# Optimization experiments

Measured on AMD Instinct MI355X. Metric: run time of the kernel, lower is better.

The kernel has to match this reference:

```python
import jax, jax.numpy as jnp
import numpy as np

HEAD_DIM = 64
K = 3              # kernel_size
DILATION = 1
SCALE = HEAD_DIM ** (-0.5)
PAD = DILATION * (K - 1) // 2


def setup_inputs() -> dict:
    key = jax.random.key(0)
    kq, kk, kv = jax.random.split(key, 3)
    shape = (8, 512, 56, 56)  # B, d, H, W
    return {
        "q": jax.random.normal(kq, shape, dtype=jnp.float32),
        "k": jax.random.normal(kk, shape, dtype=jnp.float32),
        "v": jax.random.normal(kv, shape, dtype=jnp.float32),
    }


def _unfold(x, B, h, H, W):
    # torch nn.Unfold(kernel=K, dilation=1, padding=PAD, stride=1):
    # output [B, d*K*K, H*W] with (channel, kh, kw) channel-major ordering,
    # which matches lax.conv_general_dilated_patches output layout.
    p = jax.lax.conv_general_dilated_patches(
        x, (K, K), (1, 1), ((PAD, PAD), (PAD, PAD)),
        rhs_dilation=(DILATION, DILATION),
        dimension_numbers=("NCHW", "OIHW", "NCHW"),
    )  # [B, d*K*K, H, W]
    return p.reshape(B, h, HEAD_DIM, K * K, H * W)


def reference(q, k, v):
    B, d, H, W = q.shape
    h = d // HEAD_DIM  # number of heads
    # q -> [B, h, HW, head_dim]
    qr = q.reshape(B, h, HEAD_DIM, H * W).transpose(0, 1, 3, 2)
    ku = _unfold(k, B, h, H, W)  # [B, h, hd, K*K, HW]
    vu = _unfold(v, B, h, H, W)  # [B, h, hd, K*K, HW]
    # per-pixel local attention over the K*K window
    attn = jnp.einsum("bhpc,bhckp->bhpk", qr, ku) * SCALE  # [B,h,HW,K*K]
    attn = jax.nn.softmax(attn, axis=-1)
    out = jnp.einsum("bhpk,bhckp->bhpc", attn, vu)  # [B,h,HW,hd]
    # -> [B, HW, h, hd] -> [B, H, W, d]
    return out.transpose(0, 2, 1, 3).reshape(B, H, W, d)
```

## Files before the change

kernel.cpp:

```cpp
#include <hip/hip_runtime.h>


namespace {

constexpr int HD = 64, HH = 56, WW = 56, HW = HH * WW;
constexpr int CS = HW, DTOT = 512;
constexpr float SCALE = 0.125f;
constexpr int TSTR = 36;

__device__ __forceinline__ float tapLf(float v) {
  int i = __float_as_int(v);
  return __int_as_float(__builtin_amdgcn_update_dpp(i, i, 0x138, 0xF, 0xF, false));
}
__device__ __forceinline__ float tapRf(float v) {
  int i = __float_as_int(v);
  return __int_as_float(__builtin_amdgcn_update_dpp(i, i, 0x130, 0xF, 0xF, false));
}

__global__ __launch_bounds__(64, 4)
void adda_fwd(const float* __restrict__ qg, const float* __restrict__ kg,
              const float* __restrict__ vg, float* __restrict__ outg) {
  __shared__ float tbuf[56 * TSTR];

  int wg = (int)blockIdx.x;
  const int nwg = (int)gridDim.x;
  if ((nwg & 7) == 0) wg = (wg & 7) * (nwg >> 3) + (wg >> 3);

  const int bh  = wg / 56;
  const int rem = wg - bh * 56;
  const int pair = rem >> 1;
  const int h    = rem & 1;
  const int l    = (int)threadIdx.x;
  const int r    = l >> 5;
  const int xc   = l & 31;
  const int y    = pair * 2;
  const int yown = y + r;
  const int x    = h * 28 - 1 + xc;
  const int xg   = x < 0 ? 0 : (x > WW - 1 ? WW - 1 : x);
  const int yout = r ? (y + 2 > HH - 1 ? HH - 1 : y + 2)
                     : (y > 0 ? y - 1 : 0);

  const long base = (long)bh * HD * HW;
  const float* __restrict__ qp  = qg + base + (long)yown * WW + xg;
  const float* __restrict__ kop = kg + base + (long)yown * WW + xg;
  const float* __restrict__ kxp = kg + base + (long)yout * WW + xg;
  const float* __restrict__ vop = vg + base + (long)yown * WW + xg;
  const float* __restrict__ vxp = vg + base + (long)yout * WW + xg;

  float lg[9];
#pragma unroll
  for (int n = 0; n < 9; ++n) lg[n] = 0.f;

  float koA[8], kxA[8], qqA[8];
  float koB[8], kxB[8], qqB[8];
  float voA[8], vxA[8];
  float voB[8], vxB[8];

#define LOADK(S, cb)                                    \
  _Pragma("unroll") for (int i = 0; i < 8; ++i) {       \
    qq##S[i] = qp[((cb) + i) * CS];                     \
    ko##S[i] = kop[((cb) + i) * CS];                    \
    kx##S[i] = kxp[((cb) + i) * CS];                    \
  }
#define CONSK(S)                                        \
  _Pragma("unroll") for (int i = 0; i < 8; ++i) {       \
    const float swp = __shfl_xor(ko##S[i], 32);         \
    const float abv = r ? swp : kx##S[i];               \
    const float blw = r ? kx##S[i] : swp;               \
    const float own = ko##S[i];                         \
    const float qv  = qq##S[i];                         \
    lg[0] = fmaf(qv, tapLf(abv), lg[0]);                \
    lg[1] = fmaf(qv, abv,        lg[1]);                \
    lg[2] = fmaf(qv, tapRf(abv), lg[2]);                \
    lg[3] = fmaf(qv, tapLf(own), lg[3]);                \
    lg[4] = fmaf(qv, own,        lg[4]);                \
    lg[5] = fmaf(qv, tapRf(own), lg[5]);                \
    lg[6] = fmaf(qv, tapLf(blw), lg[6]);                \
    lg[7] = fmaf(qv, blw,        lg[7]);                \
    lg[8] = fmaf(qv, tapRf(blw), lg[8]);                \
  }
#define LOADV(S, cb)                                    \
  _Pragma("unroll") for (int i = 0; i < 8; ++i) {       \
    vo##S[i] = vop[((cb) + i) * CS];                    \
    vx##S[i] = vxp[((cb) + i) * CS];                    \
  }

  LOADK(A, 0);  LOADK(B, 8);
  CONSK(A); LOADK(A, 16);
  CONSK(B); LOADK(B, 24);
  CONSK(A); LOADK(A, 32);
  CONSK(B); LOADK(B, 40);
  CONSK(A); LOADK(A, 48);
  CONSK(B); LOADK(B, 56);
  CONSK(A); LOADV(A, 0);
  CONSK(B); LOADV(B, 8);

  const bool okt = r ? true : (y > 0);
  const bool okb = r ? (y + 2 < HH) : true;
  const bool okl = x > 0;
  const bool okr = x < WW - 1;
  const bool ok[9] = {okt && okl, okt, okt && okr,
                      okl,        true, okr,
                      okb && okl, okb, okb && okr};
  float w[9];
  float mx = 0.f;
#pragma unroll
  for (int n = 0; n < 9; ++n) { w[n] = ok[n] ? lg[n] * SCALE : 0.f; mx = fmaxf(mx, w[n]); }
  float sum = 0.f;
#pragma unroll
  for (int n = 0; n < 9; ++n) { w[n] = __expf(w[n] - mx); sum += w[n]; }
  const float inv = 1.f / sum;
#pragma unroll
  for (int n = 0; n < 9; ++n) w[n] = ok[n] ? w[n] * inv : 0.f;

  const bool pxv = (xc >= 1) && (xc <= 28);
  const int pxw = r * 28 + xc - 1;

#define CONSV(S, cb)                                    \
  {                                                     \
    float o[8];                                         \
    _Pragma("unroll") for (int i = 0; i < 8; ++i) {     \
      const float swp = __shfl_xor(vo##S[i], 32);       \
      const float abv = r ? swp : vx##S[i];             \
      const float blw = r ? vx##S[i] : swp;             \
      const float own = vo##S[i];                       \
      float a = w[0] * tapLf(abv);                      \
      a = fmaf(w[1], abv,        a);                    \
      a = fmaf(w[2], tapRf(abv), a);                    \
      a = fmaf(w[3], tapLf(own), a);                    \
      a = fmaf(w[4], own,        a);                    \
      a = fmaf(w[5], tapRf(own), a);                    \
      a = fmaf(w[6], tapLf(blw), a);                    \
      a = fmaf(w[7], blw,        a);                    \
      a = fmaf(w[8], tapRf(blw), a);                    \
      o[i] = a;                                         \
    }                                                   \
    if (pxv) {                                          \
      const int cl = (cb) & 31;                         \
      *(float4*)&tbuf[pxw * TSTR + cl]     = make_float4(o[0], o[1], o[2], o[3]); \
      *(float4*)&tbuf[pxw * TSTR + cl + 4] = make_float4(o[4], o[5], o[6], o[7]); \
    }                                                   \
  }

  float* __restrict__ ob =
      outg + ((long)(bh >> 3) * HW + (long)y * WW + h * 28) * DTOT + (bh & 7) * HD;

#define READOUT(ch0)                                    \
  _Pragma("unroll") for (int rr = 0; rr < 7; ++rr) {    \
    const int g = rr * 64 + l;                          \
    const int pw = g >> 3, slot = g & 7;                \
    const int pa = pw + ((pw >= 28) ? 28 : 0);          \
    const float4 tv = *(const float4*)&tbuf[pw * TSTR + slot * 4]; \
    *(float4*)(ob + (long)pa * DTOT + (ch0) + slot * 4) = tv;      \
  }

  CONSV(A, 0);  LOADV(A, 16);
  CONSV(B, 8);  LOADV(B, 24);
  CONSV(A, 16); LOADV(A, 32);
  CONSV(B, 24); LOADV(B, 40);
  READOUT(0);
  CONSV(A, 32); LOADV(A, 48);
  CONSV(B, 40); LOADV(B, 56);
  CONSV(A, 48);
  CONSV(B, 56);
  READOUT(32);

#undef LOADK
#undef CONSK
#undef LOADV
#undef CONSV
#undef READOUT
}

}

extern "C" void kernel_launch(void* const* d_in, const int* in_sizes, int n_in,
                              void* d_out, int out_size, void* d_ws, size_t ws_size,
                              hipStream_t stream) {
  const float* q = (const float*)d_in[0];
  const float* k = (const float*)d_in[1];
  const float* v = (const float*)d_in[2];
  float* out = (float*)d_out;

  const int BH = in_sizes[0] / (HD * HW);
  dim3 grid(BH * 56);
  adda_fwd<<<grid, 64, 0, stream>>>(q, k, v, out);
}
```

Baseline: 39.21 us.

## Compute two horizontal pixels per lane with float2 loads over full-width row pairs

Each lane now owns two adjacent pixels, loaded as float2 from three rows (above, own, below) of q/k/v. Each workgroup covers a full 56-pixel row pair instead of half-row tiles with halo lanes. This drops the redundant halo loads and the cross-half shuffle, and halves the grid. The cost is doubled accumulator and weight registers (18 logits) and lower occupancy, with launch bounds reduced to 2, plus 4 of every 32 lanes idle.

```diff
diff --git a/kernel.cpp b/kernel.cpp
--- a/kernel.cpp
+++ b/kernel.cpp
@@ -6,6 +6,7 @@
 constexpr int HD = 64, HH = 56, WW = 56, HW = HH * WW;
 constexpr int CS = HW, DTOT = 512;
 constexpr float SCALE = 0.125f;
+constexpr int NP   = HH / 2;
 constexpr int TSTR = 36;
 
 __device__ __forceinline__ float tapLf(float v) {
@@ -17,72 +18,88 @@
   return __int_as_float(__builtin_amdgcn_update_dpp(i, i, 0x130, 0xF, 0xF, false));
 }
 
-__global__ __launch_bounds__(64, 4)
+__global__ __launch_bounds__(64, 2)
 void adda_fwd(const float* __restrict__ qg, const float* __restrict__ kg,
               const float* __restrict__ vg, float* __restrict__ outg) {
-  __shared__ float tbuf[56 * TSTR];
+  __shared__ float tbuf[112 * TSTR];
 
   int wg = (int)blockIdx.x;
   const int nwg = (int)gridDim.x;
   if ((nwg & 7) == 0) wg = (wg & 7) * (nwg >> 3) + (wg >> 3);
 
-  const int bh  = wg / 56;
-  const int rem = wg - bh * 56;
-  const int pair = rem >> 1;
-  const int h    = rem & 1;
+  const int pair = wg % NP;
+  const int bh   = wg / NP;
   const int l    = (int)threadIdx.x;
   const int r    = l >> 5;
-  const int xc   = l & 31;
+  const int pl   = l & 31;
+  const int p    = pl < 28 ? pl : 27;
+  const bool act = pl < 28;
   const int y    = pair * 2;
   const int yown = y + r;
-  const int x    = h * 28 - 1 + xc;
-  const int xg   = x < 0 ? 0 : (x > WW - 1 ? WW - 1 : x);
-  const int yout = r ? (y + 2 > HH - 1 ? HH - 1 : y + 2)
-                     : (y > 0 ? y - 1 : 0);
+  const int x0   = 2 * p;
 
   const long base = (long)bh * HD * HW;
-  const float* __restrict__ qp  = qg + base + (long)yown * WW + xg;
-  const float* __restrict__ kop = kg + base + (long)yown * WW + xg;
-  const float* __restrict__ kxp = kg + base + (long)yout * WW + xg;
-  const float* __restrict__ vop = vg + base + (long)yown * WW + xg;
-  const float* __restrict__ vxp = vg + base + (long)yout * WW + xg;
-
-  float lg[9];
-#pragma unroll
-  for (int n = 0; n < 9; ++n) lg[n] = 0.f;
-
-  float koA[8], kxA[8], qqA[8];
-  float koB[8], kxB[8], qqB[8];
-  float voA[8], vxA[8];
-  float voB[8], vxB[8];
+  const int rA = (yown > 0) ? yown - 1 : 0;
+  const int rC = (yown < HH - 1) ? yown + 1 : HH - 1;
+
+  const float* __restrict__ qp  = qg + base + (long)yown * WW + x0;
+  const float* __restrict__ kap = kg + base + (long)rA * WW + x0;
+  const float* __restrict__ kbp = kg + base + (long)yown * WW + x0;
+  const float* __restrict__ kcp = kg + base + (long)rC * WW + x0;
+  const float* __restrict__ vap = vg + base + (long)rA * WW + x0;
+  const float* __restrict__ vbp = vg + base + (long)yown * WW + x0;
+  const float* __restrict__ vcp = vg + base + (long)rC * WW + x0;
+
+  float lg[18];
+#pragma unroll
+  for (int n = 0; n < 18; ++n) lg[n] = 0.f;
+
+  float2 qA[8], aA[8], bA[8], cA[8];
+  float2 qB[8], aB[8], bB[8], cB[8];
 
 #define LOADK(S, cb)                                    \
   _Pragma("unroll") for (int i = 0; i < 8; ++i) {       \
-    qq##S[i] = qp[((cb) + i) * CS];                     \
-    ko##S[i] = kop[((cb) + i) * CS];                    \
-    kx##S[i] = kxp[((cb) + i) * CS];                    \
+    const int co = ((cb) + i) * CS;                     \
+    q##S[i] = *(const float2*)(qp + co);                \
+    a##S[i] = *(const float2*)(kap + co);               \
+    b##S[i] = *(const float2*)(kbp + co);               \
+    c##S[i] = *(const float2*)(kcp + co);               \
   }
 #define CONSK(S)                                        \
   _Pragma("unroll") for (int i = 0; i < 8; ++i) {       \
-    const float swp = __shfl_xor(ko##S[i], 32);         \
-    const float abv = r ? swp : kx##S[i];               \
-    const float blw = r ? kx##S[i] : swp;               \
-    const float own = ko##S[i];                         \
-    const float qv  = qq##S[i];                         \
-    lg[0] = fmaf(qv, tapLf(abv), lg[0]);                \
-    lg[1] = fmaf(qv, abv,        lg[1]);                \
-    lg[2] = fmaf(qv, tapRf(abv), lg[2]);                \
-    lg[3] = fmaf(qv, tapLf(own), lg[3]);                \
-    lg[4] = fmaf(qv, own,        lg[4]);                \
-    lg[5] = fmaf(qv, tapRf(own), lg[5]);                \
-    lg[6] = fmaf(qv, tapLf(blw), lg[6]);                \
-    lg[7] = fmaf(qv, blw,        lg[7]);                \
-    lg[8] = fmaf(qv, tapRf(blw), lg[8]);                \
-  }
+    const float2 qv = q##S[i];                          \
+    const float2 A = a##S[i], B2 = b##S[i], C = c##S[i];\
+    const float tlA = tapLf(A.y),  trA = tapRf(A.x);    \
+    const float tlB = tapLf(B2.y), trB = tapRf(B2.x);   \
+    const float tlC = tapLf(C.y),  trC = tapRf(C.x);    \
+    lg[0]  = fmaf(qv.x, tlA,  lg[0]);                   \
+    lg[1]  = fmaf(qv.x, A.x,  lg[1]);                   \
+    lg[2]  = fmaf(qv.x, A.y,  lg[2]);                   \
+    lg[3]  = fmaf(qv.x, tlB,  lg[3]);                   \
+    lg[4]  = fmaf(qv.x, B2.x, lg[4]);                   \
+    lg[5]  = fmaf(qv.x, B2.y, lg[5]);                   \
+    lg[6]  = fmaf(qv.x, tlC,  lg[6]);                   \
+    lg[7]  = fmaf(qv.x, C.x,  lg[7]);                   \
+    lg[8]  = fmaf(qv.x, C.y,  lg[8]);                   \
+    lg[9]  = fmaf(qv.y, A.x,  lg[9]);                   \
+    lg[10] = fmaf(qv.y, A.y,  lg[10]);                  \
+    lg[11] = fmaf(qv.y, trA,  lg[11]);                  \
+    lg[12] = fmaf(qv.y, B2.x, lg[12]);                  \
+    lg[13] = fmaf(qv.y, B2.y, lg[13]);                  \
+    lg[14] = fmaf(qv.y, trB,  lg[14]);                  \
+    lg[15] = fmaf(qv.y, C.x,  lg[15]);                  \
+    lg[16] = fmaf(qv.y, C.y,  lg[16]);                  \
+    lg[17] = fmaf(qv.y, trC,  lg[17]);                  \
+  }
+
+  float2 vaA[8], vbA[8], vcA[8];
+  float2 vaB[8], vbB[8], vcB[8];
 #define LOADV(S, cb)                                    \
   _Pragma("unroll") for (int i = 0; i < 8; ++i) {       \
-    vo##S[i] = vop[((cb) + i) * CS];                    \
-    vx##S[i] = vxp[((cb) + i) * CS];                    \
+    const int co = ((cb) + i) * CS;                     \
+    va##S[i] = *(const float2*)(vap + co);              \
+    vb##S[i] = *(const float2*)(vbp + co);              \
+    vc##S[i] = *(const float2*)(vcp + co);              \
   }
 
   LOADK(A, 0);  LOADK(B, 8);
@@ -95,63 +112,88 @@
   CONSK(A); LOADV(A, 0);
   CONSK(B); LOADV(B, 8);
 
-  const bool okt = r ? true : (y > 0);
-  const bool okb = r ? (y + 2 < HH) : true;
-  const bool okl = x > 0;
-  const bool okr = x < WW - 1;
-  const bool ok[9] = {okt && okl, okt, okt && okr,
-                      okl,        true, okr,
-                      okb && okl, okb, okb && okr};
-  float w[9];
-  float mx = 0.f;
-#pragma unroll
-  for (int n = 0; n < 9; ++n) { w[n] = ok[n] ? lg[n] * SCALE : 0.f; mx = fmaxf(mx, w[n]); }
-  float sum = 0.f;
-#pragma unroll
-  for (int n = 0; n < 9; ++n) { w[n] = __expf(w[n] - mx); sum += w[n]; }
-  const float inv = 1.f / sum;
-#pragma unroll
-  for (int n = 0; n < 9; ++n) w[n] = ok[n] ? w[n] * inv : 0.f;
-
-  const bool pxv = (xc >= 1) && (xc <= 28);
-  const int pxw = r * 28 + xc - 1;
-
-#define CONSV(S, cb)                                    \
+  const bool okA = (yown > 0);
+  const bool okC = (yown < HH - 1);
+  const bool okl = (p > 0);
+  const bool okr = (p < 27);
+  const bool ok0[9] = {okA && okl, okA, okA,
+                       okl,        true, true,
+                       okC && okl, okC, okC};
+  const bool ok1[9] = {okA, okA, okA && okr,
+                       true, true, okr,
+                       okC, okC, okC && okr};
+  float w[18];
+  {
+    float mx = 0.f;
+#pragma unroll
+    for (int n = 0; n < 9; ++n) { w[n] = ok0[n] ? lg[n] * SCALE : 0.f; mx = fmaxf(mx, w[n]); }
+    float sum = 0.f;
+#pragma unroll
+    for (int n = 0; n < 9; ++n) { w[n] = __expf(w[n] - mx); sum += w[n]; }
+    const float inv = 1.f / sum;
+#pragma unroll
+    for (int n = 0; n < 9; ++n) w[n] = ok0[n] ? w[n] * inv : 0.f;
+  }
+  {
+    float mx = 0.f;
+#pragma unroll
+    for (int n = 0; n < 9; ++n) { w[9 + n] = ok1[n] ? lg[9 + n] * SCALE : 0.f; mx = fmaxf(mx, w[9 + n]); }
+    float sum = 0.f;
+#pragma unroll
+    for (int n = 0; n < 9; ++n) { w[9 + n] = __expf(w[9 + n] - mx); sum += w[9 + n]; }
+    const float inv = 1.f / sum;
+#pragma unroll
+    for (int n = 0; n < 9; ++n) w[9 + n] = ok1[n] ? w[9 + n] * inv : 0.f;
+  }
+
+  const int row0 = r * 56 + x0;
+
+#define CONSV(S, cl)                                    \
   {                                                     \
-    float o[8];                                         \
+    float o0[8], o1[8];                                 \
     _Pragma("unroll") for (int i = 0; i < 8; ++i) {     \
-      const float swp = __shfl_xor(vo##S[i], 32);       \
-      const float abv = r ? swp : vx##S[i];             \
-      const float blw = r ? vx##S[i] : swp;             \
-      const float own = vo##S[i];                       \
-      float a = w[0] * tapLf(abv);                      \
-      a = fmaf(w[1], abv,        a);                    \
-      a = fmaf(w[2], tapRf(abv), a);                    \
-      a = fmaf(w[3], tapLf(own), a);                    \
-      a = fmaf(w[4], own,        a);                    \
-      a = fmaf(w[5], tapRf(own), a);                    \
-      a = fmaf(w[6], tapLf(blw), a);                    \
-      a = fmaf(w[7], blw,        a);                    \
-      a = fmaf(w[8], tapRf(blw), a);                    \
-      o[i] = a;                                         \
+      const float2 A = va##S[i], B2 = vb##S[i], C = vc##S[i]; \
+      const float tlA = tapLf(A.y),  trA = tapRf(A.x);  \
+      const float tlB = tapLf(B2.y), trB = tapRf(B2.x); \
+      const float tlC = tapLf(C.y),  trC = tapRf(C.x);  \
+      float s0 = w[0] * tlA;                            \
+      s0 = fmaf(w[1], A.x,  s0);                        \
+      s0 = fmaf(w[2], A.y,  s0);                        \
+      s0 = fmaf(w[3], tlB,  s0);                        \
+      s0 = fmaf(w[4], B2.x, s0);                        \
+      s0 = fmaf(w[5], B2.y, s0);                        \
+      s0 = fmaf(w[6], tlC,  s0);                        \
+      s0 = fmaf(w[7], C.x,  s0);                        \
+      s0 = fmaf(w[8], C.y,  s0);                        \
+      o0[i] = s0;                                       \
+      float s1 = w[9] * A.x;                            \
+      s1 = fmaf(w[10], A.y,  s1);                       \
+      s1 = fmaf(w[11], trA,  s1);                       \
+      s1 = fmaf(w[12], B2.x, s1);                       \
+      s1 = fmaf(w[13], B2.y, s1);                       \
+      s1 = fmaf(w[14], trB,  s1);                       \
+      s1 = fmaf(w[15], C.x,  s1);                       \
+      s1 = fmaf(w[16], C.y,  s1);                       \
+      s1 = fmaf(w[17], trC,  s1);                       \
+      o1[i] = s1;                                       \
     }                                                   \
-    if (pxv) {                                          \
-      const int cl = (cb) & 31;                         \
-      *(float4*)&tbuf[pxw * TSTR + cl]     = make_float4(o[0], o[1], o[2], o[3]); \
-      *(float4*)&tbuf[pxw * TSTR + cl + 4] = make_float4(o[4], o[5], o[6], o[7]); \
+    if (act) {                                          \
+      *(float4*)&tbuf[row0 * TSTR + (cl)]           = make_float4(o0[0], o0[1], o0[2], o0[3]); \
+      *(float4*)&tbuf[row0 * TSTR + (cl) + 4]       = make_float4(o0[4], o0[5], o0[6], o0[7]); \
+      *(float4*)&tbuf[(row0 + 1) * TSTR + (cl)]     = make_float4(o1[0], o1[1], o1[2], o1[3]); \
+      *(float4*)&tbuf[(row0 + 1) * TSTR + (cl) + 4] = make_float4(o1[4], o1[5], o1[6], o1[7]); \
     }                                                   \
   }
 
   float* __restrict__ ob =
-      outg + ((long)(bh >> 3) * HW + (long)y * WW + h * 28) * DTOT + (bh & 7) * HD;
+      outg + ((long)(bh >> 3) * HW + (long)y * WW) * DTOT + (bh & 7) * HD;
 
 #define READOUT(ch0)                                    \
-  _Pragma("unroll") for (int rr = 0; rr < 7; ++rr) {    \
+  _Pragma("unroll") for (int rr = 0; rr < 14; ++rr) {   \
     const int g = rr * 64 + l;                          \
-    const int pw = g >> 3, slot = g & 7;                \
-    const int pa = pw + ((pw >= 28) ? 28 : 0);          \
-    const float4 tv = *(const float4*)&tbuf[pw * TSTR + slot * 4]; \
-    *(float4*)(ob + (long)pa * DTOT + (ch0) + slot * 4) = tv;      \
+    const int pg = g >> 3, slot = g & 7;                \
+    const float4 tv = *(const float4*)&tbuf[pg * TSTR + slot * 4]; \
+    *(float4*)(ob + (long)pg * DTOT + (ch0) + slot * 4) = tv;      \
   }
 
   CONSV(A, 0);  LOADV(A, 16);
@@ -159,10 +201,10 @@
   CONSV(A, 16); LOADV(A, 32);
   CONSV(B, 24); LOADV(B, 40);
   READOUT(0);
-  CONSV(A, 32); LOADV(A, 48);
-  CONSV(B, 40); LOADV(B, 56);
-  CONSV(A, 48);
-  CONSV(B, 56);
+  CONSV(A, 0);  LOADV(A, 48);
+  CONSV(B, 8);  LOADV(B, 56);
+  CONSV(A, 16);
+  CONSV(B, 24);
   READOUT(32);
 
 #undef LOADK
@@ -183,6 +225,6 @@
   float* out = (float*)d_out;
 
   const int BH = in_sizes[0] / (HD * HW);
-  dim3 grid(BH * 56);
+  dim3 grid(BH * NP);
   adda_fwd<<<grid, 64, 0, stream>>>(q, k, v, out);
 }
```

Result: faster. 38.00 us (-3.1%).
